# Optimization experiments

Hardware: AMD Instinct MI355X
Metric: run time of the kernel (lower is better)

The kernel has to match this reference:

```python
import jax, jax.numpy as jnp
import numpy as np

B, T, C = 2, 2048, 2048
NH = 16            # query heads
NKV = NH // 2      # kv heads (GQA)
HD = C // NH       # head dim = 128
N_REP = NH // NKV  # 2


def setup_inputs() -> dict:
    key = jax.random.key(0)
    k1, k2, k3 = jax.random.split(key, 3)
    x = jax.random.normal(k1, (B, T, C), jnp.float32)
    w_attn = jax.random.normal(k2, (C, (NH + 2 * NKV) * HD), jnp.float32) * 0.02
    w_proj = jax.random.normal(k3, (C, C), jnp.float32) * 0.02
    t = jnp.arange(T, dtype=jnp.float32)
    inv_freq = 1.0 / (10000.0 ** (jnp.arange(0, HD, 2, dtype=jnp.float32) / HD))
    freqs = t[:, None] * inv_freq[None, :]  # [T, HD//2]
    return {"x": x, "w_attn": w_attn, "w_proj": w_proj,
            "freqs_cos": jnp.cos(freqs), "freqs_sin": jnp.sin(freqs)}


def _rope(v, cos, sin):
    # v: [B, T, H, HD]; complex multiply on (even, odd) pairs
    vr = v.reshape(*v.shape[:-1], HD // 2, 2)
    x0, x1 = vr[..., 0], vr[..., 1]
    c = cos[None, :, None, :]
    s = sin[None, :, None, :]
    o0 = x0 * c - x1 * s
    o1 = x0 * s + x1 * c
    return jnp.stack([o0, o1], axis=-1).reshape(v.shape)


def reference(x, w_attn, w_proj, freqs_cos, freqs_sin):
    qkv = x @ w_attn  # [B, T, (NH+2*NKV)*HD]
    q, k, v = jnp.split(qkv, [NH * HD, (NH + NKV) * HD], axis=-1)
    q = q.reshape(B, T, NH, HD)
    k = k.reshape(B, T, NKV, HD)
    v = v.reshape(B, T, NKV, HD)
    q = _rope(q, freqs_cos, freqs_sin)
    k = _rope(k, freqs_cos, freqs_sin)
    # GQA: group query heads over kv heads instead of repeating k/v
    q = q.transpose(0, 2, 1, 3).reshape(B, NKV, N_REP, T, HD)  # [B, G, R, T, HD]
    k = k.transpose(0, 2, 1, 3)  # [B, G, T, HD]
    v = v.transpose(0, 2, 1, 3)  # [B, G, T, HD]
    scale = jnp.float32(1.0 / np.sqrt(HD))
    scores = jnp.einsum('bgrqd,bgkd->bgrqk', q, k) * scale
    causal = jnp.tril(jnp.ones((T, T), dtype=bool))
    scores = jnp.where(causal, scores, jnp.float32(-1e30))
    p = jax.nn.softmax(scores, axis=-1)
    y = jnp.einsum('bgrqk,bgkd->bgrqd', p, v)  # [B, G, R, T, HD]
    y = y.reshape(B, NH, T, HD).transpose(0, 2, 1, 3).reshape(B, T, C)
    return y @ w_proj
```

## Files before the change

### kernel.cpp

```cpp
#include <hip/hip_runtime.h>
#include <hip/hip_bf16.h>
#include <stdint.h>
#include <stddef.h>

typedef unsigned short u16;
using bf16x8 = __attribute__((ext_vector_type(8))) short;
using f32x4  = __attribute__((ext_vector_type(4))) float;
using f32x16 = __attribute__((ext_vector_type(16))) float;

#define DEVFN static __device__ __forceinline__

DEVFN u16 f2b(float f){ __hip_bfloat16 h = __float2bfloat16(f); return *reinterpret_cast<u16*>(&h); }
DEVFN float b2f(u16 u){ __hip_bfloat16 h; *reinterpret_cast<u16*>(&h) = u; return __bfloat162float(h); }

DEVFN void gload_lds16(const void* g, void* l){
  __builtin_amdgcn_global_load_lds(
      (const __attribute__((address_space(1))) void*)g,
      (__attribute__((address_space(3))) void*)l, 16, 0, 0);
}

__global__ void detect_k(const uint32_t* __restrict__ fc_raw, uint32_t* __restrict__ flag){
  if (threadIdx.x == 0 && blockIdx.x == 0)
    flag[0] = (fc_raw[0] == 0x3F800000u) ? 1u : 0u;
}

__global__ __launch_bounds__(256) void cvtf_k(const void* __restrict__ in, float* __restrict__ out,
                                              int n, const uint32_t* __restrict__ flag){
  const int i = blockIdx.x*256 + threadIdx.x;
  if (i >= n) return;
  if (flag[0]) out[i] = ((const float*)in)[i];
  else         out[i] = b2f(((const u16*)in)[i]);
}

__global__ __launch_bounds__(256) void cvtx_k(const void* __restrict__ in, u16* __restrict__ out,
                                              int n8, const uint32_t* __restrict__ flag){
  const int i = blockIdx.x*256 + threadIdx.x;
  if (i >= n8) return;
  __align__(16) u16 e[8];
  if (flag[0]){
    const float* f = (const float*)in + (size_t)i*8;
    float4 a = *(const float4*)f, b = *(const float4*)(f+4);
    e[0]=f2b(a.x); e[1]=f2b(a.y); e[2]=f2b(a.z); e[3]=f2b(a.w);
    e[4]=f2b(b.x); e[5]=f2b(b.y); e[6]=f2b(b.z); e[7]=f2b(b.w);
  } else {
    *(uint4*)e = *((const uint4*)in + i);
  }
  *(uint4*)(out + (size_t)i*8) = *(const uint4*)e;
}

__global__ __launch_bounds__(512) void wtrans_k(const void* __restrict__ in, u16* __restrict__ out,
                                                int C, int R, const uint32_t* __restrict__ flag){
  __shared__ __align__(16) u16 tile[64][72];
  const int r0 = blockIdx.y*64, c0 = blockIdx.x*64;
  const int t = threadIdx.x, r = t>>3, cs = (t&7)*8;
  __align__(16) u16 e[8];
  if (flag[0]){
    const float* f = (const float*)in + (size_t)(r0+r)*C + c0 + cs;
    float4 a = *(const float4*)f, b = *(const float4*)(f+4);
    e[0]=f2b(a.x); e[1]=f2b(a.y); e[2]=f2b(a.z); e[3]=f2b(a.w);
    e[4]=f2b(b.x); e[5]=f2b(b.y); e[6]=f2b(b.z); e[7]=f2b(b.w);
  } else {
    *(uint4*)e = *(const uint4*)((const u16*)in + (size_t)(r0+r)*C + c0 + cs);
  }
#pragma unroll
  for (int j=0;j<8;j++) tile[cs+j][r] = e[j];
  __syncthreads();
  uint4 o = *(const uint4*)&tile[r][cs];
  *(uint4*)(out + (size_t)(c0+r)*R + r0 + cs) = o;
}

__global__ __launch_bounds__(512) void vtrans_k(const u16* __restrict__ qkv, u16* __restrict__ vT){
  __shared__ __align__(16) u16 tile[64][72];
  const int z = blockIdx.z, b = z>>3, g = z&7;
  const u16* in = qkv + (size_t)(b*2048)*4096 + 3072 + g*128;
  u16* out = vT + (size_t)z*128*2048;
  const int r0 = blockIdx.y*64, c0 = blockIdx.x*64;
  const int t = threadIdx.x, r = t>>3, cs = (t&7)*8;
  uint4 v = *(const uint4*)(in + (size_t)(r0+r)*4096 + c0 + cs);
  const u16* e = (const u16*)&v;
#pragma unroll
  for (int j=0;j<8;j++) tile[cs+j][r] = e[j];
  __syncthreads();
  uint4 o = *(const uint4*)&tile[r][cs];
  *(uint4*)(out + (size_t)(c0+r)*2048 + r0 + cs) = o;
}

__global__ __launch_bounds__(256) void rope_k(u16* qkv, const float* __restrict__ fc,
                                              const float* __restrict__ fs){
  const int idx = blockIdx.x*256 + threadIdx.x;
  const int row = idx / 1536;
  const int p   = idx % 1536;
  const int col0 = p*2;
  const int t = row & 2047;
  const int i = p & 63;
  uint32_t* ptr = (uint32_t*)(qkv + (size_t)row*4096 + col0);
  uint32_t u = *ptr;
  float x0 = b2f((u16)(u & 0xffff));
  float x1 = b2f((u16)(u >> 16));
  float c = fc[t*64+i], s = fs[t*64+i];
  float o0 = x0*c - x1*s;
  float o1 = x0*s + x1*c;
  *ptr = (uint32_t)f2b(o0) | ((uint32_t)f2b(o1) << 16);
}

__global__ __launch_bounds__(256) void gemm_bt(const u16* __restrict__ A, const u16* __restrict__ Bt,
                                               void* __restrict__ Cv, int M, int N, int K,
                                               const uint32_t* __restrict__ flag, int fin){
  __shared__ __align__(16) u16 Al[2][128*32];
  __shared__ __align__(16) u16 Bl[2][128*32];
  const int nwg_x = N>>7;
  int wg = blockIdx.x;
  {
    const int nwg = gridDim.x;
    const int cpx = nwg >> 3;
    wg = (wg & 7)*cpx + (wg >> 3);
  }
  const int tm = (wg / nwg_x)*128, tn = (wg % nwg_x)*128;
  const int tid = threadIdx.x, w = tid>>6, l = tid&63, lr = l&15, lg = l>>4;
  const int wr = w>>1, wc = w&1;

  f32x4 acc[4][4] = {};

  auto stage = [&](int buf, int kk){
#pragma unroll
    for (int issue=0; issue<2; ++issue){
      const int c = issue*256 + w*64 + l;
      const int r = c>>2, sl = c&3;
      const int gch = sl ^ (r&3);
      gload_lds16(A  + (size_t)(tm + r)*K + kk + gch*8, &Al[buf][(issue*256 + w*64)*8]);
      gload_lds16(Bt + (size_t)(tn + r)*K + kk + gch*8, &Bl[buf][(issue*256 + w*64)*8]);
    }
  };

  stage(0, 0);
  __syncthreads();
  const int nk = K>>5;
  for (int kt=0; kt<nk; ++kt){
    if (kt+1 < nk) stage((kt+1)&1, (kt+1)*32);
    const u16* Ab = Al[kt&1];
    const u16* Bb = Bl[kt&1];
    bf16x8 a[4], b[4];
#pragma unroll
    for (int mi=0;mi<4;mi++){
      const int rr = wr*64 + mi*16 + lr;
      a[mi] = *(const bf16x8*)&Ab[rr*32 + ((lg ^ (rr&3))*8)];
    }
#pragma unroll
    for (int ni=0;ni<4;ni++){
      const int rr = wc*64 + ni*16 + lr;
      b[ni] = *(const bf16x8*)&Bb[rr*32 + ((lg ^ (rr&3))*8)];
    }
#pragma unroll
    for (int mi=0;mi<4;mi++)
#pragma unroll
      for (int ni=0;ni<4;ni++)
        acc[mi][ni] = __builtin_amdgcn_mfma_f32_16x16x32_bf16(a[mi], b[ni], acc[mi][ni], 0,0,0);
    __syncthreads();
  }
  const bool of32 = fin && (flag[0] != 0);
#pragma unroll
  for (int mi=0;mi<4;mi++)
#pragma unroll
    for (int ni=0;ni<4;ni++)
#pragma unroll
      for (int reg=0;reg<4;reg++){
        const int row = tm + wr*64 + mi*16 + lg*4 + reg;
        const int col = tn + wc*64 + ni*16 + lr;
        const size_t idx = (size_t)row*N + col;
        const float v = acc[mi][ni][reg];
        if (of32) ((float*)Cv)[idx] = v;
        else      ((u16*)Cv)[idx]   = f2b(v);
      }
}

__global__ __launch_bounds__(512, 1) void attn_k(const u16* __restrict__ qkv,
                                                 const u16* __restrict__ vT,
                                                 u16* __restrict__ y){
  __shared__ __align__(16) u16 KV[2][2][16384];
  const int i0 = blockIdx.x;
  const int g  = i0 & 7;
  const int r1 = i0 >> 3;
  const int hl = r1 & 1;
  const int vq = (r1 >> 1) & 7;
  const int b  = r1 >> 4;
  const int h  = g*2 + hl;

  const int tid = threadIdx.x;
  const int w = tid >> 6, l = tid & 63;
  const int grp = w >> 2, wq = w & 3;
  const int lq = l & 31;
  const int hi = l >> 5;
  const float scale = 0.08838834764831845f;

  const u16* kg = qkv + (size_t)(b*2048)*4096 + 2048 + g*128;
  const u16* vg = vT  + (size_t)(b*8+g)*128*2048;

  const int rk = tid >> 2, cb = tid & 3;
  uint4 kpre[4], vpre[4];
  auto loadT = [&](int kvbase){
#pragma unroll
    for (int j=0;j<4;j++){
      const int ch = cb + j*4;
      kpre[j] = *(const uint4*)(kg + (size_t)(kvbase + rk)*4096 + ch*8);
      vpre[j] = *(const uint4*)(vg + (size_t)rk*2048 + kvbase + ch*8);
    }
  };
  auto writeT = [&](int buf){
    u16* Kd = &KV[buf][rk>>6][0];
    const int rl = rk & 63;
#pragma unroll
    for (int j=0;j<4;j++){
      const int ch = cb + j*4;
      *(uint4*)&Kd[rl*128 + ((ch ^ (rl&15))*8)] = kpre[j];
    }
#pragma unroll
    for (int j=0;j<4;j++){
      const int ch = cb + j*4;
      u16* Vd = &KV[buf][ch>>3][8192];
      *(uint4*)&Vd[rk*64 + (((ch&7) ^ (rk&7))*8)] = vpre[j];
    }
  };

  int qt = vq;
  const int nA = vq + 1;
  bf16x8 qf[8];
  f32x16 yacc[4];
  float mrow, lsum;

  auto loadQ = [&]{
    const size_t qrow = (size_t)(b*2048 + qt*128 + wq*32 + lq);
    const u16* qp = qkv + qrow*4096 + h*128 + hi*8;
#pragma unroll
    for (int ds=0; ds<8; ++ds) qf[ds] = *(const bf16x8*)(qp + ds*16);
  };
  auto resetAcc = [&]{
#pragma unroll
    for (int dt=0; dt<4; ++dt)
#pragma unroll
      for (int r=0; r<16; ++r) yacc[dt][r] = 0.f;
    mrow = -1e30f; lsum = 0.f;
  };

  auto mergePhase = [&](u16* Mb){
    float* Mm = (float*)Mb; float* Ml = Mm + 128;
    u16* MOs = Mb + 512 + wq*4096;
    __syncthreads();
    if (grp == 1){
      if (l < 32){ Mm[wq*32 + l] = mrow; Ml[wq*32 + l] = lsum; }
#pragma unroll
      for (int dt=0; dt<4; ++dt)
#pragma unroll
        for (int rq=0; rq<4; ++rq){
          const int d0 = dt*32 + rq*8 + hi*4;
          uint32_t lo = (uint32_t)f2b(yacc[dt][rq*4+0]) | ((uint32_t)f2b(yacc[dt][rq*4+1])<<16);
          uint32_t hi2= (uint32_t)f2b(yacc[dt][rq*4+2]) | ((uint32_t)f2b(yacc[dt][rq*4+3])<<16);
          const int idx = (lq*128 + d0) ^ ((lq&7)<<3);
          *(uint2*)&MOs[idx] = make_uint2(lo, hi2);
        }
    }
    __syncthreads();
    if (grp == 0){
      const float mo = Mm[wq*32 + lq], lo_ = Ml[wq*32 + lq];
      const float ms = fmaxf(mrow, mo);
      const float ce = __expf(mrow - ms), co = __expf(mo - ms);
      const float inv = 1.f / (lsum*ce + lo_*co);
#pragma unroll
      for (int dt=0; dt<4; ++dt)
#pragma unroll
        for (int rq=0; rq<4; ++rq){
          const int d0 = dt*32 + rq*8 + hi*4;
          const int idx = (lq*128 + d0) ^ ((lq&7)<<3);
          uint2 pr = *(const uint2*)&MOs[idx];
          const float yo0 = b2f((u16)(pr.x & 0xffff)), yo1 = b2f((u16)(pr.x >> 16));
          const float yo2 = b2f((u16)(pr.y & 0xffff)), yo3 = b2f((u16)(pr.y >> 16));
          const float f0 = (yacc[dt][rq*4+0]*ce + yo0*co)*inv;
          const float f1 = (yacc[dt][rq*4+1]*ce + yo1*co)*inv;
          const float f2v= (yacc[dt][rq*4+2]*ce + yo2*co)*inv;
          const float f3 = (yacc[dt][rq*4+3]*ce + yo3*co)*inv;
          uint32_t lo = (uint32_t)f2b(f0) | ((uint32_t)f2b(f1)<<16);
          uint32_t hi2= (uint32_t)f2b(f2v)| ((uint32_t)f2b(f3)<<16);
          *(uint2*)&MOs[idx] = make_uint2(lo, hi2);
        }
    }
    __syncthreads();
    const int qb2 = b*2048 + qt*128 + wq*32;
#pragma unroll
    for (int p=0; p<2; ++p){
      const int row = grp*16 + p*8 + (l>>3);
      const int gc = l & 7;
      const int idx0 = (row*128 + gc*16) ^ ((row&7)<<3);
      const int idx1 = (row*128 + gc*16 + 8) ^ ((row&7)<<3);
      uint4 v0 = *(const uint4*)&MOs[idx0];
      uint4 v1 = *(const uint4*)&MOs[idx1];
      u16* yp = y + (size_t)(qb2 + row)*2048 + h*128 + gc*16;
      *(uint4*)yp = v0;
      *(uint4*)(yp + 8) = v1;
    }
    __syncthreads();
  };

  loadT(0); writeT(0); __syncthreads();
  loadQ(); resetAcc();

  for (int s=0; s<17; ++s){
    if (s == nA){
      mergePhase(&KV[(nA&1)^1][0][0]);
      qt = 15 - vq;
      loadQ(); resetAcc();
    }
    const int sj = (s < nA) ? s : s - nA;
    const int kvbase = sj*128;
    if (s+1 < 17){
      const int s2 = s+1;
      const int sj2 = (s2 < nA) ? s2 : s2 - nA;
      loadT(sj2*128);
    }
    const u16* Kb = &KV[s&1][grp][0];
    const u16* Vb = Kb + 8192;
    const int tilebase = kvbase + grp*64;
    const int qmin = qt*128 + wq*32;
    const int qrow = qmin + lq;

    if (tilebase <= qmin + 31){
      f32x16 sc[2];
#pragma unroll
      for (int t=0;t<2;t++)
#pragma unroll
        for (int r=0;r<16;r++) sc[t][r] = 0.f;
      __builtin_amdgcn_s_setprio(1);
#pragma unroll
      for (int t=0; t<2; ++t){
        const int r = t*32 + lq;
        const int rsw = r & 15;
#pragma unroll
        for (int ds=0; ds<8; ++ds){
          const bf16x8 kf = *(const bf16x8*)&Kb[r*128 + (((2*ds+hi) ^ rsw)*8)];
          sc[t] = __builtin_amdgcn_mfma_f32_32x32x16_bf16(kf, qf[ds], sc[t], 0,0,0);
        }
      }
      __builtin_amdgcn_s_setprio(0);

      const bool needmask = (tilebase + 63) > qmin;
      float pmax = -1e30f;
#pragma unroll
      for (int t=0;t<2;t++)
#pragma unroll
        for (int r=0;r<16;r++){
          float v = sc[t][r]*scale;
          if (needmask){
            const int kp = tilebase + t*32 + (r&3) + 8*(r>>2) + 4*hi;
            if (kp > qrow) v = -1e30f;
          }
          sc[t][r] = v;
          pmax = fmaxf(pmax, v);
        }
      pmax = fmaxf(pmax, __shfl_xor(pmax, 32));
      if (!__all(pmax <= mrow + 8.f)){
        const float mnew = fmaxf(mrow, pmax);
        const float corr = __expf(mrow - mnew);
        mrow = mnew; lsum *= corr;
#pragma unroll
        for (int dt=0;dt<4;dt++)
#pragma unroll
          for (int r=0;r<16;r++) yacc[dt][r] *= corr;
      }
      float lsub = 0.f;
#pragma unroll
      for (int t=0;t<2;t++)
#pragma unroll
        for (int r=0;r<16;r++){
          const float p = __expf(sc[t][r] - mrow);
          sc[t][r] = p; lsub += p;
        }
      lsub += __shfl_xor(lsub, 32);
      lsum += lsub;

      __align__(16) uint32_t pw[4][4];
#pragma unroll
      for (int t=0;t<2;t++)
#pragma unroll
        for (int half=0; half<2; ++half){
          const int q8 = half*8;
          uint32_t X0 = (uint32_t)f2b(sc[t][q8+0]) | ((uint32_t)f2b(sc[t][q8+1])<<16);
          uint32_t X1 = (uint32_t)f2b(sc[t][q8+2]) | ((uint32_t)f2b(sc[t][q8+3])<<16);
          uint32_t X2 = (uint32_t)f2b(sc[t][q8+4]) | ((uint32_t)f2b(sc[t][q8+5])<<16);
          uint32_t X3 = (uint32_t)f2b(sc[t][q8+6]) | ((uint32_t)f2b(sc[t][q8+7])<<16);
          const uint32_t pX0 = (uint32_t)__shfl_xor((int)X0, 32);
          const uint32_t pX1 = (uint32_t)__shfl_xor((int)X1, 32);
          const uint32_t pX2 = (uint32_t)__shfl_xor((int)X2, 32);
          const uint32_t pX3 = (uint32_t)__shfl_xor((int)X3, 32);
          const int ks = t*2 + half;
          pw[ks][0] = hi ? pX2 : X0;
          pw[ks][1] = hi ? pX3 : X1;
          pw[ks][2] = hi ? X2 : pX0;
          pw[ks][3] = hi ? X3 : pX1;
        }

      __builtin_amdgcn_s_setprio(1);
#pragma unroll
      for (int dt=0; dt<4; ++dt){
        const int d = dt*32 + lq;
        const int dsw = d & 7;
#pragma unroll
        for (int ks=0; ks<4; ++ks){
          const bf16x8 vf = *(const bf16x8*)&Vb[d*64 + (((2*ks+hi) ^ dsw)*8)];
          yacc[dt] = __builtin_amdgcn_mfma_f32_32x32x16_bf16(vf, *(const bf16x8*)&pw[ks][0], yacc[dt], 0,0,0);
        }
      }
      __builtin_amdgcn_s_setprio(0);
    }

    if (s+1 < 17) writeT((s&1)^1);
    __syncthreads();
  }
  mergePhase(&KV[0][0][0]);
}

extern "C" void kernel_launch(void* const* d_in, const int* in_sizes, int n_in,
                              void* d_out, int out_size, void* d_ws, size_t ws_size,
                              hipStream_t stream){
  char* ws = (char*)d_ws;
  const size_t MB = 1048576;
  uint32_t* flag = (uint32_t*)(ws);
  float* fcF = (float*)(ws + 1*MB);
  float* fsF = (float*)(ws + 1*MB + 524288);
  u16* xb   = (u16*)(ws + 2*MB);
  u16* waT  = (u16*)(ws + 18*MB);
  u16* wpT  = (u16*)(ws + 34*MB);
  u16* qkvb = (u16*)(ws + 42*MB);
  u16* vTb  = (u16*)(ws + 74*MB);
  u16* yb   = xb;

  detect_k<<<1, 64, 0, stream>>>((const uint32_t*)d_in[3], flag);
  cvtf_k  <<<512, 256, 0, stream>>>(d_in[3], fcF, 131072, flag);
  cvtf_k  <<<512, 256, 0, stream>>>(d_in[4], fsF, 131072, flag);
  cvtx_k  <<<4096, 256, 0, stream>>>(d_in[0], xb, 1048576, flag);
  wtrans_k<<<dim3(64,32,1), 512, 0, stream>>>(d_in[1], waT, 4096, 2048, flag);
  wtrans_k<<<dim3(32,32,1), 512, 0, stream>>>(d_in[2], wpT, 2048, 2048, flag);
  gemm_bt <<<dim3(1024,1,1), 256, 0, stream>>>(xb, waT, qkvb, 4096, 4096, 2048, flag, 0);
  rope_k  <<<dim3(24576,1,1), 256, 0, stream>>>(qkvb, fcF, fsF);
  vtrans_k<<<dim3(2,32,16), 512, 0, stream>>>(qkvb, vTb);
  attn_k  <<<dim3(256,1,1), 512, 0, stream>>>(qkvb, vTb, yb);
  gemm_bt <<<dim3(512,1,1), 256, 0, stream>>>(yb, wpT, d_out, 4096, 2048, 2048, flag, 1);
}
```

Measured before the change: 304.1 us.

## Restructure attention into independent per-wave query tiles reading K/V directly from global

Replaces the 512-thread attention block, which shared double-buffered K/V tiles in LDS and split the KV range across two wave groups with an LDS merge, with 256-thread blocks. In these, each wave independently processes a 32-row query tile (paired with its mirrored tile for causal balance) and loads K and V fragments straight from global memory. It also folds the softmax scale and log2(e) into Q during RoPE and uses the raw v_exp_f32 (exp2) instruction. This removes LDS staging, barriers and the cross-group merge, but relies on L2/cache for K/V reuse and may expose global load latency in the MFMA loop.

```diff
diff --git a/kernel.cpp b/kernel.cpp
--- a/kernel.cpp
+++ b/kernel.cpp
@@ -12,6 +12,7 @@
 
 DEVFN u16 f2b(float f){ __hip_bfloat16 h = __float2bfloat16(f); return *reinterpret_cast<u16*>(&h); }
 DEVFN float b2f(u16 u){ __hip_bfloat16 h; *reinterpret_cast<u16*>(&h) = u; return __bfloat162float(h); }
+DEVFN float ex2(float x){ float r; asm("v_exp_f32 %0, %1" : "=v"(r) : "v"(x)); return r; }
 
 DEVFN void gload_lds16(const void* g, void* l){
   __builtin_amdgcn_global_load_lds(
@@ -100,6 +101,10 @@
   float c = fc[t*64+i], s = fs[t*64+i];
   float o0 = x0*c - x1*s;
   float o1 = x0*s + x1*c;
+  if (col0 < 2048){
+    const float SCL = 0.08838834764831845f * 1.4426950408889634f;
+    o0 *= SCL; o1 *= SCL;
+  }
   *ptr = (uint32_t)f2b(o0) | ((uint32_t)f2b(o1) << 16);
 }
 
@@ -173,155 +178,48 @@
       }
 }
 
-__global__ __launch_bounds__(512, 1) void attn_k(const u16* __restrict__ qkv,
+__global__ __launch_bounds__(256, 1) void attn_k(const u16* __restrict__ qkv,
                                                  const u16* __restrict__ vT,
                                                  u16* __restrict__ y){
-  __shared__ __align__(16) u16 KV[2][2][16384];
   const int i0 = blockIdx.x;
   const int g  = i0 & 7;
-  const int r1 = i0 >> 3;
-  const int hl = r1 & 1;
-  const int vq = (r1 >> 1) & 7;
-  const int b  = r1 >> 4;
+  const int j  = i0 >> 3;
+  const int w  = threadIdx.x >> 6;
+  const int l  = threadIdx.x & 63;
+  const int lq = l & 31, hi = l >> 5;
+  const int jj = j*4 + w;
+  const int v  = jj & 31;
+  const int hl = (jj >> 5) & 1;
+  const int b  = jj >> 6;
   const int h  = g*2 + hl;
-
-  const int tid = threadIdx.x;
-  const int w = tid >> 6, l = tid & 63;
-  const int grp = w >> 2, wq = w & 3;
-  const int lq = l & 31;
-  const int hi = l >> 5;
-  const float scale = 0.08838834764831845f;
 
   const u16* kg = qkv + (size_t)(b*2048)*4096 + 2048 + g*128;
   const u16* vg = vT  + (size_t)(b*8+g)*128*2048;
 
-  const int rk = tid >> 2, cb = tid & 3;
-  uint4 kpre[4], vpre[4];
-  auto loadT = [&](int kvbase){
-#pragma unroll
-    for (int j=0;j<4;j++){
-      const int ch = cb + j*4;
-      kpre[j] = *(const uint4*)(kg + (size_t)(kvbase + rk)*4096 + ch*8);
-      vpre[j] = *(const uint4*)(vg + (size_t)rk*2048 + kvbase + ch*8);
-    }
-  };
-  auto writeT = [&](int buf){
-    u16* Kd = &KV[buf][rk>>6][0];
-    const int rl = rk & 63;
-#pragma unroll
-    for (int j=0;j<4;j++){
-      const int ch = cb + j*4;
-      *(uint4*)&Kd[rl*128 + ((ch ^ (rl&15))*8)] = kpre[j];
-    }
-#pragma unroll
-    for (int j=0;j<4;j++){
-      const int ch = cb + j*4;
-      u16* Vd = &KV[buf][ch>>3][8192];
-      *(uint4*)&Vd[rk*64 + (((ch&7) ^ (rk&7))*8)] = vpre[j];
-    }
-  };
-
-  int qt = vq;
-  const int nA = vq + 1;
-  bf16x8 qf[8];
-  f32x16 yacc[4];
-  float mrow, lsum;
-
-  auto loadQ = [&]{
-    const size_t qrow = (size_t)(b*2048 + qt*128 + wq*32 + lq);
-    const u16* qp = qkv + qrow*4096 + h*128 + hi*8;
-#pragma unroll
-    for (int ds=0; ds<8; ++ds) qf[ds] = *(const bf16x8*)(qp + ds*16);
-  };
-  auto resetAcc = [&]{
+#pragma unroll 1
+  for (int ph=0; ph<2; ++ph){
+    const int qt   = ph ? (63 - v) : v;
+    const int nkt  = (qt>>1) + 1;
+    const int qmin = qt*32;
+    const int qrow = qmin + lq;
+
+    bf16x8 qf[8];
+    {
+      const u16* qp = qkv + (size_t)(b*2048 + qmin + lq)*4096 + h*128 + hi*8;
+#pragma unroll
+      for (int ds=0; ds<8; ++ds) qf[ds] = *(const bf16x8*)(qp + ds*16);
+    }
+    f32x16 yacc[4];
 #pragma unroll
     for (int dt=0; dt<4; ++dt)
 #pragma unroll
       for (int r=0; r<16; ++r) yacc[dt][r] = 0.f;
-    mrow = -1e30f; lsum = 0.f;
-  };
-
-  auto mergePhase = [&](u16* Mb){
-    float* Mm = (float*)Mb; float* Ml = Mm + 128;
-    u16* MOs = Mb + 512 + wq*4096;
-    __syncthreads();
-    if (grp == 1){
-      if (l < 32){ Mm[wq*32 + l] = mrow; Ml[wq*32 + l] = lsum; }
-#pragma unroll
-      for (int dt=0; dt<4; ++dt)
-#pragma unroll
-        for (int rq=0; rq<4; ++rq){
-          const int d0 = dt*32 + rq*8 + hi*4;
-          uint32_t lo = (uint32_t)f2b(yacc[dt][rq*4+0]) | ((uint32_t)f2b(yacc[dt][rq*4+1])<<16);
-          uint32_t hi2= (uint32_t)f2b(yacc[dt][rq*4+2]) | ((uint32_t)f2b(yacc[dt][rq*4+3])<<16);
-          const int idx = (lq*128 + d0) ^ ((lq&7)<<3);
-          *(uint2*)&MOs[idx] = make_uint2(lo, hi2);
-        }
-    }
-    __syncthreads();
-    if (grp == 0){
-      const float mo = Mm[wq*32 + lq], lo_ = Ml[wq*32 + lq];
-      const float ms = fmaxf(mrow, mo);
-      const float ce = __expf(mrow - ms), co = __expf(mo - ms);
-      const float inv = 1.f / (lsum*ce + lo_*co);
-#pragma unroll
-      for (int dt=0; dt<4; ++dt)
-#pragma unroll
-        for (int rq=0; rq<4; ++rq){
-          const int d0 = dt*32 + rq*8 + hi*4;
-          const int idx = (lq*128 + d0) ^ ((lq&7)<<3);
-          uint2 pr = *(const uint2*)&MOs[idx];
-          const float yo0 = b2f((u16)(pr.x & 0xffff)), yo1 = b2f((u16)(pr.x >> 16));
-          const float yo2 = b2f((u16)(pr.y & 0xffff)), yo3 = b2f((u16)(pr.y >> 16));
-          const float f0 = (yacc[dt][rq*4+0]*ce + yo0*co)*inv;
-          const float f1 = (yacc[dt][rq*4+1]*ce + yo1*co)*inv;
-          const float f2v= (yacc[dt][rq*4+2]*ce + yo2*co)*inv;
-          const float f3 = (yacc[dt][rq*4+3]*ce + yo3*co)*inv;
-          uint32_t lo = (uint32_t)f2b(f0) | ((uint32_t)f2b(f1)<<16);
-          uint32_t hi2= (uint32_t)f2b(f2v)| ((uint32_t)f2b(f3)<<16);
-          *(uint2*)&MOs[idx] = make_uint2(lo, hi2);
-        }
-    }
-    __syncthreads();
-    const int qb2 = b*2048 + qt*128 + wq*32;
-#pragma unroll
-    for (int p=0; p<2; ++p){
-      const int row = grp*16 + p*8 + (l>>3);
-      const int gc = l & 7;
-      const int idx0 = (row*128 + gc*16) ^ ((row&7)<<3);
-      const int idx1 = (row*128 + gc*16 + 8) ^ ((row&7)<<3);
-      uint4 v0 = *(const uint4*)&MOs[idx0];
-      uint4 v1 = *(const uint4*)&MOs[idx1];
-      u16* yp = y + (size_t)(qb2 + row)*2048 + h*128 + gc*16;
-      *(uint4*)yp = v0;
-      *(uint4*)(yp + 8) = v1;
-    }
-    __syncthreads();
-  };
-
-  loadT(0); writeT(0); __syncthreads();
-  loadQ(); resetAcc();
-
-  for (int s=0; s<17; ++s){
-    if (s == nA){
-      mergePhase(&KV[(nA&1)^1][0][0]);
-      qt = 15 - vq;
-      loadQ(); resetAcc();
-    }
-    const int sj = (s < nA) ? s : s - nA;
-    const int kvbase = sj*128;
-    if (s+1 < 17){
-      const int s2 = s+1;
-      const int sj2 = (s2 < nA) ? s2 : s2 - nA;
-      loadT(sj2*128);
-    }
-    const u16* Kb = &KV[s&1][grp][0];
-    const u16* Vb = Kb + 8192;
-    const int tilebase = kvbase + grp*64;
-    const int qmin = qt*128 + wq*32;
-    const int qrow = qmin + lq;
-
-    if (tilebase <= qmin + 31){
+    float mrow = -1e30f, lsum = 0.f;
+
+#pragma unroll 1
+    for (int kt=0; kt<nkt; ++kt){
+      const int kbase = kt*64;
+
       f32x16 sc[2];
 #pragma unroll
       for (int t=0;t<2;t++)
@@ -330,34 +228,33 @@
       __builtin_amdgcn_s_setprio(1);
 #pragma unroll
       for (int t=0; t<2; ++t){
-        const int r = t*32 + lq;
-        const int rsw = r & 15;
+        const u16* kp = kg + (size_t)(kbase + t*32 + lq)*4096 + hi*8;
 #pragma unroll
         for (int ds=0; ds<8; ++ds){
-          const bf16x8 kf = *(const bf16x8*)&Kb[r*128 + (((2*ds+hi) ^ rsw)*8)];
+          const bf16x8 kf = *(const bf16x8*)(kp + ds*16);
           sc[t] = __builtin_amdgcn_mfma_f32_32x32x16_bf16(kf, qf[ds], sc[t], 0,0,0);
         }
       }
       __builtin_amdgcn_s_setprio(0);
 
-      const bool needmask = (tilebase + 63) > qmin;
+      const bool needmask = (kbase + 63) > qmin;
       float pmax = -1e30f;
 #pragma unroll
       for (int t=0;t<2;t++)
 #pragma unroll
         for (int r=0;r<16;r++){
-          float v = sc[t][r]*scale;
+          float vv = sc[t][r];
           if (needmask){
-            const int kp = tilebase + t*32 + (r&3) + 8*(r>>2) + 4*hi;
-            if (kp > qrow) v = -1e30f;
+            const int kp2 = kbase + t*32 + (r&3) + 8*(r>>2) + 4*hi;
+            if (kp2 > qrow) vv = -1e30f;
           }
-          sc[t][r] = v;
-          pmax = fmaxf(pmax, v);
+          sc[t][r] = vv;
+          pmax = fmaxf(pmax, vv);
         }
       pmax = fmaxf(pmax, __shfl_xor(pmax, 32));
       if (!__all(pmax <= mrow + 8.f)){
         const float mnew = fmaxf(mrow, pmax);
-        const float corr = __expf(mrow - mnew);
+        const float corr = ex2(mrow - mnew);
         mrow = mnew; lsum *= corr;
 #pragma unroll
         for (int dt=0;dt<4;dt++)
@@ -369,7 +266,7 @@
       for (int t=0;t<2;t++)
 #pragma unroll
         for (int r=0;r<16;r++){
-          const float p = __expf(sc[t][r] - mrow);
+          const float p = ex2(sc[t][r] - mrow);
           sc[t][r] = p; lsub += p;
         }
       lsub += __shfl_xor(lsub, 32);
@@ -399,21 +296,28 @@
       __builtin_amdgcn_s_setprio(1);
 #pragma unroll
       for (int dt=0; dt<4; ++dt){
-        const int d = dt*32 + lq;
-        const int dsw = d & 7;
+        const u16* vp = vg + (size_t)(dt*32 + lq)*2048 + kbase + hi*8;
 #pragma unroll
         for (int ks=0; ks<4; ++ks){
-          const bf16x8 vf = *(const bf16x8*)&Vb[d*64 + (((2*ks+hi) ^ dsw)*8)];
+          const bf16x8 vf = *(const bf16x8*)(vp + ks*16);
           yacc[dt] = __builtin_amdgcn_mfma_f32_32x32x16_bf16(vf, *(const bf16x8*)&pw[ks][0], yacc[dt], 0,0,0);
         }
       }
       __builtin_amdgcn_s_setprio(0);
     }
 
-    if (s+1 < 17) writeT((s&1)^1);
-    __syncthreads();
-  }
-  mergePhase(&KV[0][0][0]);
+    const float inv = 1.f / lsum;
+    u16* yp = y + (size_t)(b*2048 + qmin + lq)*2048 + h*128;
+#pragma unroll
+    for (int dt=0; dt<4; ++dt)
+#pragma unroll
+      for (int rq=0; rq<4; ++rq){
+        const int d0 = dt*32 + rq*8 + hi*4;
+        uint32_t lo = (uint32_t)f2b(yacc[dt][rq*4+0]*inv) | ((uint32_t)f2b(yacc[dt][rq*4+1]*inv)<<16);
+        uint32_t hi2= (uint32_t)f2b(yacc[dt][rq*4+2]*inv) | ((uint32_t)f2b(yacc[dt][rq*4+3]*inv)<<16);
+        *(uint2*)(yp + d0) = make_uint2(lo, hi2);
+      }
+  }
 }
 
 extern "C" void kernel_launch(void* const* d_in, const int* in_sizes, int n_in,
@@ -440,6 +344,6 @@
   gemm_bt <<<dim3(1024,1,1), 256, 0, stream>>>(xb, waT, qkvb, 4096, 4096, 2048, flag, 0);
   rope_k  <<<dim3(24576,1,1), 256, 0, stream>>>(qkvb, fcF, fsF);
   vtrans_k<<<dim3(2,32,16), 512, 0, stream>>>(qkvb, vTb);
-  attn_k  <<<dim3(256,1,1), 512, 0, stream>>>(qkvb, vTb, yb);
+  attn_k  <<<dim3(256,1,1), 256, 0, stream>>>(qkvb, vTb, yb);
   gemm_bt <<<dim3(512,1,1), 256, 0, stream>>>(yb, wpT, d_out, 4096, 2048, 2048, flag, 1);
 }
```

Result: slower. 363.4 us (+19.5%).

## Halve attention tiles to 64 rows and double the block count

Applied to the files above, without the earlier changes.

The attention kernel moves from 512-thread blocks with 128-row query and KV tiles to 256-thread blocks with 64-row tiles, and launches 512 blocks instead of 256. The causal pairing of query tiles and the KV loop (33 steps) are rescaled to match, and shared memory drops to two 32 KB buffers so more blocks can share a CU. This aims at better occupancy and load balance across the CUs. In exchange it adds an extra barrier per step and halves the MFMA work per barrier, and the merge phase contains a redundant duplicate load.

```diff
diff --git a/kernel.cpp b/kernel.cpp
--- a/kernel.cpp
+++ b/kernel.cpp
@@ -173,63 +173,60 @@
       }
 }
 
-__global__ __launch_bounds__(512, 1) void attn_k(const u16* __restrict__ qkv,
-                                                 const u16* __restrict__ vT,
-                                                 u16* __restrict__ y){
-  __shared__ __align__(16) u16 KV[2][2][16384];
+__global__ __launch_bounds__(256) void attn_k(const u16* __restrict__ qkv,
+                                              const u16* __restrict__ vT,
+                                              u16* __restrict__ y){
+  __shared__ __align__(16) u16 KV[2][16384];
   const int i0 = blockIdx.x;
   const int g  = i0 & 7;
   const int r1 = i0 >> 3;
   const int hl = r1 & 1;
-  const int vq = (r1 >> 1) & 7;
-  const int b  = r1 >> 4;
+  const int v  = (r1 >> 1) & 15;
+  const int b  = r1 >> 5;
   const int h  = g*2 + hl;
 
   const int tid = threadIdx.x;
   const int w = tid >> 6, l = tid & 63;
-  const int grp = w >> 2, wq = w & 3;
-  const int lq = l & 31;
-  const int hi = l >> 5;
+  const int grp = w >> 1, wq = w & 1;
+  const int lq = l & 31, hi = l >> 5;
   const float scale = 0.08838834764831845f;
 
   const u16* kg = qkv + (size_t)(b*2048)*4096 + 2048 + g*128;
   const u16* vg = vT  + (size_t)(b*8+g)*128*2048;
 
   const int rk = tid >> 2, cb = tid & 3;
+  const int dv = tid >> 1, vb = (tid & 1)*4;
   uint4 kpre[4], vpre[4];
   auto loadT = [&](int kvbase){
 #pragma unroll
     for (int j=0;j<4;j++){
-      const int ch = cb + j*4;
-      kpre[j] = *(const uint4*)(kg + (size_t)(kvbase + rk)*4096 + ch*8);
-      vpre[j] = *(const uint4*)(vg + (size_t)rk*2048 + kvbase + ch*8);
+      kpre[j] = *(const uint4*)(kg + (size_t)(kvbase + rk)*4096 + (cb + j*4)*8);
+      vpre[j] = *(const uint4*)(vg + (size_t)dv*2048 + kvbase + (vb + j)*8);
     }
   };
   auto writeT = [&](int buf){
-    u16* Kd = &KV[buf][rk>>6][0];
-    const int rl = rk & 63;
+    u16* Kd = &KV[buf][0];
+    u16* Vd = &KV[buf][8192];
 #pragma unroll
     for (int j=0;j<4;j++){
       const int ch = cb + j*4;
-      *(uint4*)&Kd[rl*128 + ((ch ^ (rl&15))*8)] = kpre[j];
+      *(uint4*)&Kd[rk*128 + ((ch ^ (rk&15))*8)] = kpre[j];
     }
 #pragma unroll
     for (int j=0;j<4;j++){
-      const int ch = cb + j*4;
-      u16* Vd = &KV[buf][ch>>3][8192];
-      *(uint4*)&Vd[rk*64 + (((ch&7) ^ (rk&7))*8)] = vpre[j];
-    }
-  };
-
-  int qt = vq;
-  const int nA = vq + 1;
+      const int ch = vb + j;
+      *(uint4*)&Vd[dv*64 + ((ch ^ (dv&7))*8)] = vpre[j];
+    }
+  };
+
+  int qt = v;
+  const int nA = v + 1;
   bf16x8 qf[8];
   f32x16 yacc[4];
   float mrow, lsum;
 
   auto loadQ = [&]{
-    const size_t qrow = (size_t)(b*2048 + qt*128 + wq*32 + lq);
-    const u16* qp = qkv + qrow*4096 + h*128 + hi*8;
+    const u16* qp = qkv + (size_t)(b*2048 + qt*64 + wq*32 + lq)*4096 + h*128 + hi*8;
 #pragma unroll
     for (int ds=0; ds<8; ++ds) qf[ds] = *(const bf16x8*)(qp + ds*16);
   };
@@ -242,8 +239,8 @@
   };
 
   auto mergePhase = [&](u16* Mb){
-    float* Mm = (float*)Mb; float* Ml = Mm + 128;
-    u16* MOs = Mb + 512 + wq*4096;
+    float* Mm = (float*)Mb; float* Ml = Mm + 64;
+    u16* MOs = Mb + 256 + wq*4096;
     __syncthreads();
     if (grp == 1){
       if (l < 32){ Mm[wq*32 + l] = mrow; Ml[wq*32 + l] = lsum; }
@@ -283,15 +280,16 @@
         }
     }
     __syncthreads();
-    const int qb2 = b*2048 + qt*128 + wq*32;
+    const int qb2 = b*2048 + qt*64 + wq*32;
 #pragma unroll
     for (int p=0; p<2; ++p){
       const int row = grp*16 + p*8 + (l>>3);
       const int gc = l & 7;
       const int idx0 = (row*128 + gc*16) ^ ((row&7)<<3);
       const int idx1 = (row*128 + gc*16 + 8) ^ ((row&7)<<3);
-      uint4 v0 = *(const uint4*)&MOs[idx0];
+      uint4 v0 = *(const uint4*)&MOs[idx0 - wq*4096 + wq*4096];
       uint4 v1 = *(const uint4*)&MOs[idx1];
+      v0 = *(const uint4*)&MOs[idx0];
       u16* yp = y + (size_t)(qb2 + row)*2048 + h*128 + gc*16;
       *(uint4*)yp = v0;
       *(uint4*)(yp + 8) = v1;
@@ -302,58 +300,53 @@
   loadT(0); writeT(0); __syncthreads();
   loadQ(); resetAcc();
 
-  for (int s=0; s<17; ++s){
+  for (int s=0; s<33; ++s){
     if (s == nA){
-      mergePhase(&KV[(nA&1)^1][0][0]);
-      qt = 15 - vq;
+      mergePhase(&KV[(nA&1)^1][0]);
+      qt = 31 - v;
       loadQ(); resetAcc();
     }
     const int sj = (s < nA) ? s : s - nA;
-    const int kvbase = sj*128;
-    if (s+1 < 17){
+    const int kvbase = sj*64;
+    if (s+1 < 33){
       const int s2 = s+1;
       const int sj2 = (s2 < nA) ? s2 : s2 - nA;
-      loadT(sj2*128);
-    }
-    const u16* Kb = &KV[s&1][grp][0];
-    const u16* Vb = Kb + 8192;
-    const int tilebase = kvbase + grp*64;
-    const int qmin = qt*128 + wq*32;
+      loadT(sj2*64);
+    }
+    const u16* Kb = &KV[s&1][0];
+    const u16* Vb = &KV[s&1][8192];
+    const int tilebase = kvbase + grp*32;
+    const int qmin = qt*64 + wq*32;
     const int qrow = qmin + lq;
 
     if (tilebase <= qmin + 31){
-      f32x16 sc[2];
-#pragma unroll
-      for (int t=0;t<2;t++)
-#pragma unroll
-        for (int r=0;r<16;r++) sc[t][r] = 0.f;
+      f32x16 sc;
+#pragma unroll
+      for (int r=0;r<16;r++) sc[r] = 0.f;
       __builtin_amdgcn_s_setprio(1);
-#pragma unroll
-      for (int t=0; t<2; ++t){
-        const int r = t*32 + lq;
+      {
+        const int r = grp*32 + lq;
         const int rsw = r & 15;
 #pragma unroll
         for (int ds=0; ds<8; ++ds){
           const bf16x8 kf = *(const bf16x8*)&Kb[r*128 + (((2*ds+hi) ^ rsw)*8)];
-          sc[t] = __builtin_amdgcn_mfma_f32_32x32x16_bf16(kf, qf[ds], sc[t], 0,0,0);
+          sc = __builtin_amdgcn_mfma_f32_32x32x16_bf16(kf, qf[ds], sc, 0,0,0);
         }
       }
       __builtin_amdgcn_s_setprio(0);
 
-      const bool needmask = (tilebase + 63) > qmin;
+      const bool needmask = (tilebase + 31) > qmin;
       float pmax = -1e30f;
 #pragma unroll
-      for (int t=0;t<2;t++)
-#pragma unroll
-        for (int r=0;r<16;r++){
-          float v = sc[t][r]*scale;
-          if (needmask){
-            const int kp = tilebase + t*32 + (r&3) + 8*(r>>2) + 4*hi;
-            if (kp > qrow) v = -1e30f;
-          }
-          sc[t][r] = v;
-          pmax = fmaxf(pmax, v);
+      for (int r=0;r<16;r++){
+        float vv = sc[r]*scale;
+        if (needmask){
+          const int kp2 = tilebase + (r&3) + 8*(r>>2) + 4*hi;
+          if (kp2 > qrow) vv = -1e30f;
         }
+        sc[r] = vv;
+        pmax = fmaxf(pmax, vv);
+      }
       pmax = fmaxf(pmax, __shfl_xor(pmax, 32));
       if (!__all(pmax <= mrow + 8.f)){
         const float mnew = fmaxf(mrow, pmax);
@@ -366,35 +359,30 @@
       }
       float lsub = 0.f;
 #pragma unroll
-      for (int t=0;t<2;t++)
-#pragma unroll
-        for (int r=0;r<16;r++){
-          const float p = __expf(sc[t][r] - mrow);
-          sc[t][r] = p; lsub += p;
-        }
+      for (int r=0;r<16;r++){
+        const float p = __expf(sc[r] - mrow);
+        sc[r] = p; lsub += p;
+      }
       lsub += __shfl_xor(lsub, 32);
       lsum += lsub;
 
-      __align__(16) uint32_t pw[4][4];
-#pragma unroll
-      for (int t=0;t<2;t++)
-#pragma unroll
-        for (int half=0; half<2; ++half){
-          const int q8 = half*8;
-          uint32_t X0 = (uint32_t)f2b(sc[t][q8+0]) | ((uint32_t)f2b(sc[t][q8+1])<<16);
-          uint32_t X1 = (uint32_t)f2b(sc[t][q8+2]) | ((uint32_t)f2b(sc[t][q8+3])<<16);
-          uint32_t X2 = (uint32_t)f2b(sc[t][q8+4]) | ((uint32_t)f2b(sc[t][q8+5])<<16);
-          uint32_t X3 = (uint32_t)f2b(sc[t][q8+6]) | ((uint32_t)f2b(sc[t][q8+7])<<16);
-          const uint32_t pX0 = (uint32_t)__shfl_xor((int)X0, 32);
-          const uint32_t pX1 = (uint32_t)__shfl_xor((int)X1, 32);
-          const uint32_t pX2 = (uint32_t)__shfl_xor((int)X2, 32);
-          const uint32_t pX3 = (uint32_t)__shfl_xor((int)X3, 32);
-          const int ks = t*2 + half;
-          pw[ks][0] = hi ? pX2 : X0;
-          pw[ks][1] = hi ? pX3 : X1;
-          pw[ks][2] = hi ? X2 : pX0;
-          pw[ks][3] = hi ? X3 : pX1;
-        }
+      __align__(16) uint32_t pw[2][4];
+#pragma unroll
+      for (int half=0; half<2; ++half){
+        const int q8 = half*8;
+        uint32_t X0 = (uint32_t)f2b(sc[q8+0]) | ((uint32_t)f2b(sc[q8+1])<<16);
+        uint32_t X1 = (uint32_t)f2b(sc[q8+2]) | ((uint32_t)f2b(sc[q8+3])<<16);
+        uint32_t X2 = (uint32_t)f2b(sc[q8+4]) | ((uint32_t)f2b(sc[q8+5])<<16);
+        uint32_t X3 = (uint32_t)f2b(sc[q8+6]) | ((uint32_t)f2b(sc[q8+7])<<16);
+        const uint32_t pX0 = (uint32_t)__shfl_xor((int)X0, 32);
+        const uint32_t pX1 = (uint32_t)__shfl_xor((int)X1, 32);
+        const uint32_t pX2 = (uint32_t)__shfl_xor((int)X2, 32);
+        const uint32_t pX3 = (uint32_t)__shfl_xor((int)X3, 32);
+        pw[half][0] = hi ? pX2 : X0;
+        pw[half][1] = hi ? pX3 : X1;
+        pw[half][2] = hi ? X2 : pX0;
+        pw[half][3] = hi ? X3 : pX1;
+      }
 
       __builtin_amdgcn_s_setprio(1);
 #pragma unroll
@@ -402,18 +390,20 @@
         const int d = dt*32 + lq;
         const int dsw = d & 7;
 #pragma unroll
-        for (int ks=0; ks<4; ++ks){
-          const bf16x8 vf = *(const bf16x8*)&Vb[d*64 + (((2*ks+hi) ^ dsw)*8)];
+        for (int ks=0; ks<2; ++ks){
+          const int ch = grp*4 + ks*2 + hi;
+          const bf16x8 vf = *(const bf16x8*)&Vb[d*64 + ((ch ^ dsw)*8)];
           yacc[dt] = __builtin_amdgcn_mfma_f32_32x32x16_bf16(vf, *(const bf16x8*)&pw[ks][0], yacc[dt], 0,0,0);
         }
       }
       __builtin_amdgcn_s_setprio(0);
     }
 
-    if (s+1 < 17) writeT((s&1)^1);
+    __syncthreads();
+    if (s+1 < 33) writeT((s&1)^1);
     __syncthreads();
   }
-  mergePhase(&KV[0][0][0]);
+  mergePhase(&KV[0][0]);
 }
 
 extern "C" void kernel_launch(void* const* d_in, const int* in_sizes, int n_in,
@@ -440,6 +430,6 @@
   gemm_bt <<<dim3(1024,1,1), 256, 0, stream>>>(xb, waT, qkvb, 4096, 4096, 2048, flag, 0);
   rope_k  <<<dim3(24576,1,1), 256, 0, stream>>>(qkvb, fcF, fsF);
   vtrans_k<<<dim3(2,32,16), 512, 0, stream>>>(qkvb, vTb);
-  attn_k  <<<dim3(256,1,1), 512, 0, stream>>>(qkvb, vTb, yb);
+  attn_k  <<<dim3(512,1,1), 256, 0, stream>>>(qkvb, vTb, yb);
   gemm_bt <<<dim3(512,1,1), 256, 0, stream>>>(yb, wpT, d_out, 4096, 2048, 2048, flag, 1);
 }
```

Result: slower. 391.0 us (+28.6%).
